# Kernel optimization log

Hardware: AMD Instinct MI355X
Metric: run time of the kernel (lower is better)

Reference implementation:

```python
import jax, jax.numpy as jnp
import numpy as np

N_HEADS, N_LEVELS, N_POINTS, D_MODEL = 8, 3, 12, 64
PARAM_NAMES = ['vp0_w','vp0_b','vp1_w','vp1_b','so0_w','so0_b','so1_w','so1_b','so2_w','so2_b','so3_w','so3_b','aw0_w','aw0_b','aw1_w','aw1_b','aw2_w','aw2_b','aw3_w','aw3_b','op0_w','op0_b','op1_w','op1_b']

def _lrelu(x):
    return jnp.where(x >= 0, x, 0.1 * x)

def _conv(x, w, b):
    y = jax.lax.conv_general_dilated(x, w, (1, 1), 'SAME', dimension_numbers=('NCHW', 'OIHW', 'NCHW'))
    return y + b[None, :, None, None]

def _bilinear(img, px, py):
    # img [B,C,H,W]; px,py [B,Q] absolute pixel coords; zero padding (grid_sample 'zeros')
    B, C, H, W = img.shape
    flat = img.reshape(B, C, H * W)
    x0 = jnp.floor(px); y0 = jnp.floor(py)
    wx1 = px - x0; wy1 = py - y0
    def g(xi, yi, wgt):
        valid = (xi >= 0) & (xi <= W - 1) & (yi >= 0) & (yi <= H - 1)
        xi_c = jnp.clip(xi, 0, W - 1).astype(jnp.int32)
        yi_c = jnp.clip(yi, 0, H - 1).astype(jnp.int32)
        v = jnp.take_along_axis(flat, (yi_c * W + xi_c)[:, None, :], axis=2)
        return v * (wgt * valid)[:, None, :]
    return (g(x0, y0, (1 - wx1) * (1 - wy1)) + g(x0 + 1, y0, wx1 * (1 - wy1))
          + g(x0, y0 + 1, (1 - wx1) * wy1) + g(x0 + 1, y0 + 1, wx1 * wy1))

def _flow_warp(img, flow):
    # img [n,C,h,w]; flow [n,2,h,w] (x,y); matches grid_sample align_corners=True
    n, C, h, w = img.shape
    gy, gx = jnp.meshgrid(jnp.arange(h, dtype=img.dtype), jnp.arange(w, dtype=img.dtype), indexing='ij')
    px = (gx[None] + flow[:, 0]).reshape(n, h * w)
    py = (gy[None] + flow[:, 1]).reshape(n, h * w)
    return _bilinear(img, px, py).reshape(n, C, h, w)

def _forward(x, flow_1, flow_2, flip_flow_1, flip_flow_2, p):
    n, t, c, h, w = x.shape
    hw = h * w; THW = t * hw
    M, L, P, D = N_HEADS, N_LEVELS, N_POINTS, c // N_HEADS
    flow_cn1 = flow_1
    flow_cn2 = flow_1 + _flow_warp(flow_2, flow_1)
    flow_n1c, flow_n1n2 = flip_flow_1, flow_2
    flow_n2n1 = flip_flow_2
    flow_n2c = flip_flow_2 + _flow_warp(flip_flow_1, flip_flow_2)
    warp_cn1 = _flow_warp(x[:, 1], flow_cn1)
    warp_cn2 = _flow_warp(x[:, 2], flow_cn2)
    warp_n1c = _flow_warp(x[:, 0], flow_n1c)
    warp_n1n2 = _flow_warp(x[:, 2], flow_n1n2)
    warp_n2n1 = _flow_warp(x[:, 1], flow_n2n1)
    warp_n2c = _flow_warp(x[:, 0], flow_n2c)
    extra = jnp.concatenate([x[:, 0], warp_cn1, warp_cn2, warp_n1c, warp_n1n2, warp_n2n1, warp_n2c,
                             flow_cn1, flow_cn2, flow_n1c, flow_n1n2, flow_n2n1, flow_n2c], axis=1)
    value = _conv(_lrelu(_conv(x.reshape(n, t * c, h, w), p['vp0_w'], p['vp0_b'])), p['vp1_w'], p['vp1_b'])
    def head(e, pre):
        y = _lrelu(_conv(e, p[pre + '0_w'], p[pre + '0_b']))
        y = _lrelu(_conv(y, p[pre + '1_w'], p[pre + '1_b']))
        y = _lrelu(_conv(y, p[pre + '2_w'], p[pre + '2_b']))
        return _conv(y, p[pre + '3_w'], p[pre + '3_b'])
    so = head(extra, 'so')  # [n, L*M*L*P*2, h, w]
    aw = head(extra, 'aw')  # [n, L*M*L*P*9, h, w]
    so = so.reshape(n, t, -1, hw).transpose(0, 1, 3, 2).reshape(n, THW, M, L, P, 2)
    aw = aw.reshape(n, t, -1, hw).transpose(0, 1, 3, 2).reshape(n, THW, M, L * P * 9)
    aw = jax.nn.softmax(aw, axis=-1).reshape(n, THW, M, L, P * 9)
    # flow-guided offsets: add per-(query-frame, target-level) flow to learned offsets
    off = so.reshape(n, t, hw, M, L, P, 2)
    fz = jnp.zeros_like(flow_cn2)
    def lvl(f0, f1, f2):
        s = jnp.stack([f0, f1, f2], 1)  # [n,3,2,h,w]
        return s.transpose(0, 3, 4, 1, 2).reshape(n, hw, L, 2)[:, None, :, None, :, None, :]
    off = jnp.concatenate([
        off[:, 0:1] + lvl(fz, flow_cn1, flow_cn2),
        off[:, 1:2] + lvl(flow_n1c, fz, flow_n1n2),
        off[:, 2:3] + lvl(flow_n2c, flow_n2n1, fz)], axis=1).reshape(n, THW, M, L, P, 2)
    # 3x3 integer patch around each sampling point
    pi, pj = jnp.meshgrid(jnp.arange(-1, 2), jnp.arange(-1, 2), indexing='ij')
    patch = jnp.stack([pi, pj], -1).reshape(1, 1, 1, 1, 1, 9, 2).astype(off.dtype)
    off = (off[..., None, :] + patch).reshape(n, THW, M, L, P * 9, 2)
    # reference points (valid_ratios are all 1: full masks are zeros)
    ry, rx = jnp.meshgrid((jnp.arange(h) + 0.5) / h, (jnp.arange(w) + 0.5) / w, indexing='ij')
    ref = jnp.stack([rx, ry], -1).reshape(1, hw, 2).astype(off.dtype)
    ref = jnp.tile(ref, (1, t, 1))  # [1, THW, 2]
    norm = jnp.array([w, h], dtype=off.dtype)
    loc = ref[:, :, None, None, None, :] + off / norm  # [n,THW,M,L,P*9,2] normalized
    # multi-scale deformable attention (all L levels share (h,w)); align_corners=False, zeros pad
    P9 = P * 9
    v = value.reshape(n, t, c, hw).transpose(0, 1, 3, 2).reshape(n, THW, M, D)
    vl = v.reshape(n, L, hw, M, D).transpose(0, 3, 1, 4, 2).reshape(n * M * L, D, h, w)
    px = (loc[..., 0] * w - 0.5).transpose(0, 2, 3, 1, 4).reshape(n * M * L, THW * P9)
    py = (loc[..., 1] * h - 0.5).transpose(0, 2, 3, 1, 4).reshape(n * M * L, THW * P9)
    sampled = _bilinear(vl, px, py).reshape(n, M, L, D, THW, P9)
    out = jnp.einsum('nmldqp,nqmlp->nqmd', sampled, aw).reshape(n, THW, c)
    out = out.reshape(n, t, h, w, c).transpose(0, 1, 4, 2, 3).reshape(n, t * c, h, w)
    out = _conv(_lrelu(_conv(out, p['op0_w'], p['op0_b'])), p['op1_w'], p['op1_b'])
    return out.reshape(n, t, c, h, w) + x

def setup_inputs():
    key = jax.random.key(0)
    n, t, c, h, w = 1, 3, 64, 32, 32
    ks = jax.random.split(key, 24)
    d = {}
    d['x'] = jax.random.normal(ks[0], (n, t, c, h, w), jnp.float32)
    for i, name in enumerate(['flow_1', 'flow_2', 'flip_flow_1', 'flip_flow_2']):
        d[name] = jax.random.normal(ks[1 + i], (n, 2, h, w), jnp.float32)
    cin_extra = 7 * c + 12
    specs = [('vp0', t * c, t * c), ('vp1', t * c, t * c),
             ('so0', c, cin_extra), ('so1', c, c), ('so2', c, c), ('so3', N_LEVELS * N_HEADS * N_LEVELS * N_POINTS * 2, c),
             ('aw0', c, cin_extra), ('aw1', c, c), ('aw2', c, c), ('aw3', N_LEVELS * N_HEADS * N_LEVELS * N_POINTS * 9, c),
             ('op0', t * c, t * c), ('op1', t * c, t * c)]
    for i, (name, co, ci) in enumerate(specs):
        kw, kb = jax.random.split(ks[5 + i])
        std = (2.0 / (ci * 9)) ** 0.5
        d[name + '_w'] = jax.random.normal(kw, (co, ci, 3, 3), jnp.float32) * std
        d[name + '_b'] = jax.random.normal(kb, (co,), jnp.float32) * 0.01
    return d

def reference(x, flow_1, flow_2, flip_flow_1, flip_flow_2, vp0_w, vp0_b, vp1_w, vp1_b, so0_w, so0_b, so1_w, so1_b, so2_w, so2_b, so3_w, so3_b, aw0_w, aw0_b, aw1_w, aw1_b, aw2_w, aw2_b, aw3_w, aw3_b, op0_w, op0_b, op1_w, op1_b):
    p = dict(zip(PARAM_NAMES, (vp0_w, vp0_b, vp1_w, vp1_b, so0_w, so0_b, so1_w, so1_b, so2_w, so2_b, so3_w, so3_b, aw0_w, aw0_b, aw1_w, aw1_b, aw2_w, aw2_b, aw3_w, aw3_b, op0_w, op0_b, op1_w, op1_b)))
    return _forward(x, flow_1, flow_2, flip_flow_1, flip_flow_2, p)
```

## Files before the change

### kernel.cpp

```cpp
#include <hip/hip_runtime.h>
#include <math.h>

#define HW 1024

typedef __attribute__((ext_vector_type(8))) short bf16x8;
typedef __attribute__((ext_vector_type(4))) float floatx4;

__device__ __forceinline__ unsigned short f2bf(float f) {
    unsigned u = __float_as_uint(f);
    u += 0x7FFF + ((u >> 16) & 1);
    return (unsigned short)(u >> 16);
}
__device__ __forceinline__ float bf2f(unsigned short u) {
    return __uint_as_float(((unsigned)u) << 16);
}
__device__ __forceinline__ float bflo(unsigned u) { return __uint_as_float(u << 16); }
__device__ __forceinline__ float bfhi(unsigned u) { return __uint_as_float(u & 0xffff0000u); }

__device__ __forceinline__ float bilin32(const float* __restrict__ img, float px, float py) {
    float x0f = floorf(px), y0f = floorf(py);
    float wx = px - x0f, wy = py - y0f;
    bool vx0 = (x0f >= 0.f) && (x0f <= 31.f);
    bool vx1 = (x0f >= -1.f) && (x0f <= 30.f);
    bool vy0 = (y0f >= 0.f) && (y0f <= 31.f);
    bool vy1 = (y0f >= -1.f) && (y0f <= 30.f);
    int ix0 = (int)fminf(fmaxf(x0f, 0.f), 31.f);
    int iy0 = (int)fminf(fmaxf(y0f, 0.f), 31.f);
    int ix1 = (int)fminf(fmaxf(x0f + 1.f, 0.f), 31.f);
    int iy1 = (int)fminf(fmaxf(y0f + 1.f, 0.f), 31.f);
    float w00 = (1.f - wx) * (1.f - wy) * ((vx0 && vy0) ? 1.f : 0.f);
    float w01 = wx * (1.f - wy) * ((vx1 && vy0) ? 1.f : 0.f);
    float w10 = (1.f - wx) * wy * ((vx0 && vy1) ? 1.f : 0.f);
    float w11 = wx * wy * ((vx1 && vy1) ? 1.f : 0.f);
    return w00 * img[iy0 * 32 + ix0] + w01 * img[iy0 * 32 + ix1] +
           w10 * img[iy1 * 32 + ix0] + w11 * img[iy1 * 32 + ix1];
}

__device__ __forceinline__ float2 comp_flow(const float* __restrict__ fa,
                                            const float* __restrict__ fb, int pix) {
    int y = pix >> 5, x = pix & 31;
    float fx = fa[pix], fy = fa[HW + pix];
    float px = (float)x + fx, py = (float)y + fy;
    float2 r;
    r.x = fx + bilin32(fb, px, py);
    r.y = fy + bilin32(fb + HW, px, py);
    return r;
}

struct WD { const float* src; int cout, Cin, nCb, wbase, beg; };

__device__ __forceinline__ void wxform_tile(const WD w, int local,
                                            unsigned short* __restrict__ wgt, char* smraw) {
    float* wlds = (float*)smraw;
    const int tid = threadIdx.x;
    int co16 = local / w.nCb, cb = local - co16 * w.nCb;
    int cr0 = co16 * 16, ci0 = cb * 32;
    for (int i = tid; i < 16 * 288; i += 256) {
        int cr = i / 288, o = i - cr * 288;
        int crg = cr0 + cr, ci = ci0 + o / 9;
        float v = (crg < w.cout && ci < w.Cin)
            ? w.src[((size_t)crg * w.Cin + ci0) * 9 + o] : 0.f;
        wlds[i] = v;
    }
    __syncthreads();
    for (int e = tid; e < 9 * 512; e += 256) {
        int t = e >> 9, idx = e & 511;
        int j = idx & 7, lane = idx >> 3, q = lane >> 4, mm = lane & 15;
        wgt[((size_t)w.wbase + ((size_t)co16 * 9 + t) * w.nCb + cb) * 512 + idx] =
            f2bf(wlds[mm * 288 + (q * 8 + j) * 9 + t]);
    }
}

struct PrepP {
    const float *x, *f1, *f2, *ff1, *ff2;
    float *fcn2, *fn2c;
    unsigned short *x_pad, *extra_pad, *wgt;
    WD wd[4];
};

__global__ __launch_bounds__(256) void prep_k(PrepP P) {
    __shared__ __align__(16) char sm[16 * 288 * 4];
    const int b = blockIdx.x, tid = threadIdx.x;
    if (b < 192) {
        int idx = b * 256 + tid;
        int pix = idx / 48, c4 = idx - pix * 48;
        int y = pix >> 5, xx = pix & 31;
        int c0 = c4 * 4;
        ushort4 s;
        s.x = f2bf(P.x[(size_t)(c0 + 0) * HW + pix]);
        s.y = f2bf(P.x[(size_t)(c0 + 1) * HW + pix]);
        s.z = f2bf(P.x[(size_t)(c0 + 2) * HW + pix]);
        s.w = f2bf(P.x[(size_t)(c0 + 3) * HW + pix]);
        *(ushort4*)(&P.x_pad[(size_t)((y + 1) * 34 + xx + 1) * 192 + c0]) = s;
    } else if (b < 672) {
        int idx = (b - 192) * 256 + tid;
        int pix = idx / 120, c4 = idx - pix * 120;
        int y = pix >> 5, xx = pix & 31;
        int c0 = c4 * 4;
        float va[4];
        if (c0 < 64) {
#pragma unroll
            for (int k = 0; k < 4; ++k) va[k] = P.x[(size_t)(c0 + k) * HW + pix];
        } else if (c0 < 448) {
            int grp = (c0 - 64) >> 6;
            int c = (c0 - 64) & 63;
            const float* src; float fx, fy;
            if (grp == 0)      { src = P.x + 64 * HW;  fx = P.f1[pix];  fy = P.f1[HW + pix]; }
            else if (grp == 1) { src = P.x + 128 * HW; float2 r = comp_flow(P.f1, P.f2, pix);  fx = r.x; fy = r.y; }
            else if (grp == 2) { src = P.x;            fx = P.ff1[pix]; fy = P.ff1[HW + pix]; }
            else if (grp == 3) { src = P.x + 128 * HW; fx = P.f2[pix];  fy = P.f2[HW + pix]; }
            else if (grp == 4) { src = P.x + 64 * HW;  fx = P.ff2[pix]; fy = P.ff2[HW + pix]; }
            else               { src = P.x;            float2 r = comp_flow(P.ff2, P.ff1, pix); fx = r.x; fy = r.y; }
            float px = (float)xx + fx, py = (float)y + fy;
            float x0f = floorf(px), y0f = floorf(py);
            float wx = px - x0f, wy = py - y0f;
            bool vx0 = (x0f >= 0.f) && (x0f <= 31.f);
            bool vx1 = (x0f >= -1.f) && (x0f <= 30.f);
            bool vy0 = (y0f >= 0.f) && (y0f <= 31.f);
            bool vy1 = (y0f >= -1.f) && (y0f <= 30.f);
            int ix0 = (int)fminf(fmaxf(x0f, 0.f), 31.f);
            int iy0 = (int)fminf(fmaxf(y0f, 0.f), 31.f);
            int ix1 = (int)fminf(fmaxf(x0f + 1.f, 0.f), 31.f);
            int iy1 = (int)fminf(fmaxf(y0f + 1.f, 0.f), 31.f);
            float w00 = (1.f - wx) * (1.f - wy) * ((vx0 && vy0) ? 1.f : 0.f);
            float w01 = wx * (1.f - wy) * ((vx1 && vy0) ? 1.f : 0.f);
            float w10 = (1.f - wx) * wy * ((vx0 && vy1) ? 1.f : 0.f);
            float w11 = wx * wy * ((vx1 && vy1) ? 1.f : 0.f);
            int p00 = iy0 * 32 + ix0, p01 = iy0 * 32 + ix1;
            int p10 = iy1 * 32 + ix0, p11 = iy1 * 32 + ix1;
            const float* im = src + (size_t)c * HW;
#pragma unroll
            for (int k = 0; k < 4; ++k) {
                va[k] = w00 * im[p00] + w01 * im[p01] + w10 * im[p10] + w11 * im[p11];
                im += HW;
            }
        } else {
#pragma unroll
            for (int k = 0; k < 4; ++k) {
                int ch = c0 + k;
                float v = 0.f;
                if (ch < 460) {
                    int fc = ch - 448;
                    int which = fc >> 1, comp = fc & 1;
                    if (which == 0)      v = P.f1[comp * HW + pix];
                    else if (which == 1) { float2 r = comp_flow(P.f1, P.f2, pix);  v = comp ? r.y : r.x; }
                    else if (which == 2) v = P.ff1[comp * HW + pix];
                    else if (which == 3) v = P.f2[comp * HW + pix];
                    else if (which == 4) v = P.ff2[comp * HW + pix];
                    else                 { float2 r = comp_flow(P.ff2, P.ff1, pix); v = comp ? r.y : r.x; }
                }
                va[k] = v;
            }
        }
        ushort4 s;
        s.x = f2bf(va[0]); s.y = f2bf(va[1]); s.z = f2bf(va[2]); s.w = f2bf(va[3]);
        *(ushort4*)(&P.extra_pad[(size_t)((y + 1) * 34 + xx + 1) * 480 + c0]) = s;
    } else if (b < 688) {
        int idx = (b - 672) * 256 + tid;
        if (idx < 1024) {
            float2 r = comp_flow(P.f1, P.f2, idx);
            P.fcn2[idx] = r.x; P.fcn2[HW + idx] = r.y;
        } else if (idx < 2048) {
            int pix = idx - 1024;
            float2 r = comp_flow(P.ff2, P.ff1, pix);
            P.fn2c[pix] = r.x; P.fn2c[HW + pix] = r.y;
        }
    } else if (b < 704) {
        const int chans[9] = {192, 192, 480, 64, 64, 64, 64, 192, 192};
        size_t offs[9]; size_t a = 0;
        for (int i = 0; i < 9; ++i) { offs[i] = a; a += (size_t)1156 * chans[i]; }
        int bb = b - 688;
        for (int item = bb; item < 9 * 132; item += 16) {
            int buf = item / 132, i = item - buf * 132;
            int py, px;
            if (i < 34) { py = 0; px = i; }
            else if (i < 68) { py = 33; px = i - 34; }
            else { int j = i - 68; py = 1 + (j >> 1); px = (j & 1) ? 33 : 0; }
            int C = chans[buf];
            unsigned short* p = P.x_pad + offs[buf] + (size_t)(py * 34 + px) * C;
            for (int c = tid; c < C; c += 256) p[c] = 0;
        }
    } else {
        int blk = b - 704;
        int di = 0;
        while (di < 3 && blk >= P.wd[di + 1].beg) ++di;
        wxform_tile(P.wd[di], blk - P.wd[di].beg, P.wgt, sm);
    }
}

struct CDesc {
    const unsigned short* in;
    const unsigned short* wgt;
    const float* bias;
    void* out;
    const float* residual;
    int Cpad, nCb, Cout, mode, cmod, relu, Mblocks;
};
struct CParam {
    CDesc d[4];
    WD rwd[4];
    int rbeg[5];
    int nr;
    int ride_bx0;
    unsigned short* wgt;
};

template<int PIXROWS, int COBLK>
__device__ __forceinline__ void conv_tile(const CDesc d, int bx, int by, char* smraw) {
    constexpr int TROWS = PIXROWS + 2;
    constexpr int TC = TROWS * 34 * 4;
    constexpr int ITRIPS = (TC + 255) / 256;
    constexpr int NTY = PIXROWS / 4;
    constexpr int NACC = NTY * 2;
    constexpr int MT = COBLK / 16;
    constexpr int WN = MT * 9 * 64;
    constexpr int WTRIPS = (WN + 255) / 256;
    unsigned short* blds = (unsigned short*)smraw;
    unsigned short* wlds = (unsigned short*)(smraw + TROWS * 34 * 40 * 2);

    const int tid = threadIdx.x;
    const int w = tid >> 6, lane = tid & 63;
    const int lq = lane >> 4, ln = lane & 15;
    const int co0 = bx * COBLK;
    const int y0 = by * PIXROWS;
    const unsigned short* __restrict__ in = d.in;
    const unsigned short* __restrict__ wg = d.wgt;
    const int Cpad = d.Cpad, nCb = d.nCb;

    floatx4 acc[MT][NACC];
#pragma unroll
    for (int mt = 0; mt < MT; ++mt)
#pragma unroll
        for (int nt = 0; nt < NACC; ++nt)
            acc[mt][nt] = (floatx4){0.f, 0.f, 0.f, 0.f};

    bf16x8 ireg[ITRIPS];
    bf16x8 wreg[WTRIPS];

    auto load_regs = [&](int cb) {
        const int ci0 = cb << 5;
#pragma unroll
        for (int k = 0; k < ITRIPS; ++k) {
            int i = tid + k * 256;
            if (i < TC) {
                int r = i / 136, rem = i - r * 136, c = rem >> 2, g = rem & 3;
                ireg[k] = *(const bf16x8*)(in + (size_t)((y0 + r) * 34 + c) * Cpad + ci0 + g * 8);
            }
        }
#pragma unroll
        for (int k = 0; k < WTRIPS; ++k) {
            int i = tid + k * 256;
            if (i < WN) {
                int chunk = i >> 6, l16 = i & 63;
                int mt = chunk / 9, t = chunk - mt * 9;
                wreg[k] = *(const bf16x8*)(wg + ((size_t)(((co0 >> 4) + mt) * 9 + t) * nCb + cb) * 512 + l16 * 8);
            }
        }
    };

    load_regs(0);

    for (int cb = 0; cb < nCb; ++cb) {
        __syncthreads();
#pragma unroll
        for (int k = 0; k < ITRIPS; ++k) {
            int i = tid + k * 256;
            if (i < TC) {
                int r = i / 136, rem = i - r * 136, c = rem >> 2, g = rem & 3;
                *(bf16x8*)(&blds[(r * 34 + c) * 40 + g * 8]) = ireg[k];
            }
        }
#pragma unroll
        for (int k = 0; k < WTRIPS; ++k) {
            int i = tid + k * 256;
            if (i < WN) {
                int chunk = i >> 6, l16 = i & 63;
                *(bf16x8*)(&wlds[chunk * 512 + l16 * 8]) = wreg[k];
            }
        }
        __syncthreads();
        if (cb + 1 < nCb) load_regs(cb + 1);
        for (int t = 0; t < 9; ++t) {
            const int dy = t / 3, dx = t - dy * 3;
            bf16x8 bfr[NACC];
#pragma unroll
            for (int ty = 0; ty < NTY; ++ty)
#pragma unroll
                for (int tx = 0; tx < 2; ++tx) {
                    int yy = w * NTY + ty + dy;
                    int xx = tx * 16 + ln + dx;
                    bfr[ty * 2 + tx] = *(const bf16x8*)(&blds[(yy * 34 + xx) * 40 + lq * 8]);
                }
#pragma unroll
            for (int mt = 0; mt < MT; ++mt) {
                bf16x8 afr = *(const bf16x8*)(&wlds[(mt * 9 + t) * 512 + lane * 8]);
#pragma unroll
                for (int nt = 0; nt < NACC; ++nt)
                    acc[mt][nt] = __builtin_amdgcn_mfma_f32_16x16x32_bf16(afr, bfr[nt], acc[mt][nt], 0, 0, 0);
            }
        }
    }

#pragma unroll
    for (int mt = 0; mt < MT; ++mt) {
        const int co = co0 + mt * 16 + lq * 4;
        if (co >= d.Cout) continue;
        float bv[4];
#pragma unroll
        for (int r = 0; r < 4; ++r) bv[r] = d.bias[co + r];
#pragma unroll
        for (int nt = 0; nt < NACC; ++nt) {
            const int ty = nt >> 1, tx = nt & 1;
            const int pix = by * (PIXROWS * 32) + (w * NTY + ty) * 32 + tx * 16 + ln;
            float v[4];
#pragma unroll
            for (int r = 0; r < 4; ++r) {
                float vv = acc[mt][nt][r] + bv[r];
                if (d.relu) vv = (vv >= 0.f) ? vv : 0.1f * vv;
                v[r] = vv;
            }
            if (d.mode == 0) {
                float* o = (float*)d.out;
#pragma unroll
                for (int r = 0; r < 4; ++r) {
                    float vv = v[r];
                    if (d.residual) vv += d.residual[(size_t)(co + r) * HW + pix];
                    o[(size_t)(co + r) * HW + pix] = vv;
                }
            } else if (d.mode == 1) {
                int fq = co / d.cmod, cc = co - fq * d.cmod;
                *(float4*)((float*)d.out + ((size_t)fq * HW + pix) * d.cmod + cc) =
                    make_float4(v[0], v[1], v[2], v[3]);
            } else if (d.mode == 2) {
                int fq = co / d.cmod, cc = co - fq * d.cmod;
                ushort4 s4;
                s4.x = f2bf(v[0]); s4.y = f2bf(v[1]); s4.z = f2bf(v[2]); s4.w = f2bf(v[3]);
                *(ushort4*)((unsigned short*)d.out + ((size_t)fq * HW + pix) * d.cmod + cc) = s4;
            } else {
                int yy = (pix >> 5) + 1, xx = (pix & 31) + 1;
                ushort4 s4;
                s4.x = f2bf(v[0]); s4.y = f2bf(v[1]); s4.z = f2bf(v[2]); s4.w = f2bf(v[3]);
                *(ushort4*)((unsigned short*)d.out + (size_t)(yy * 34 + xx) * d.cmod + co) = s4;
            }
        }
    }
}

template<int PIXROWS, int COBLK>
__global__ __launch_bounds__(256) void conv_mfma_k(CParam P) {
    constexpr int TROWS = PIXROWS + 2;
    constexpr int MT = COBLK / 16;
    constexpr int SMB = TROWS * 34 * 40 * 2 + MT * 9 * 512 * 2;
    __shared__ __align__(16) char sm[(SMB > 18432) ? SMB : 18432];
    int bx = blockIdx.x;
    if (P.nr > 0 && bx >= P.ride_bx0) {
        int slot = (bx - P.ride_bx0) * gridDim.y + blockIdx.y;
        if (slot >= P.rbeg[P.nr]) return;
        int di = 0;
        while (di + 1 < P.nr && slot >= P.rbeg[di + 1]) ++di;
        wxform_tile(P.rwd[di], slot - P.rbeg[di], P.wgt, sm);
        return;
    }
    int di = 0;
    while (bx >= P.d[di].Mblocks) { bx -= P.d[di].Mblocks; ++di; }
    conv_tile<PIXROWS, COBLK>(P.d[di], bx, blockIdx.y, sm);
}

__global__ __launch_bounds__(256) void deform_attn_k(
    const unsigned short* __restrict__ value_b, const float* __restrict__ so_t,
    const unsigned short* __restrict__ aw_t,
    const float* __restrict__ flow_1, const float* __restrict__ flow_2,
    const float* __restrict__ flip_flow_1, const float* __restrict__ flip_flow_2,
    const float* __restrict__ flow_cn2, const float* __restrict__ flow_n2c,
    unsigned short* __restrict__ attn_pad)
{
    __shared__ unsigned short vlds[24576];
    __shared__ unsigned short pwlds[4][432];
    const int tid = threadIdx.x;
    const int wav = tid >> 6, lane = tid & 63;
    const int m = blockIdx.x & 7, qc = blockIdx.x >> 3;

    for (int i = tid; i < 3072; i += 256) {
        int l = i >> 10, p = i & 1023;
        *(bf16x8*)(&vlds[(size_t)i * 8]) =
            *(const bf16x8*)(value_b + ((size_t)((l * 8 + m) * 1024) + p) * 8);
    }
    __syncthreads();

    const int pp = lane & 15, gq = lane >> 4;
    const int gdy = (gq >> 1) * 2 - 1;
    const int gdx = (gq & 1) * 2 - 1;
    const bool selx = (gq & 1);
    const bool sely = (gq >> 1);

    float av[6];
    {
        const unsigned short* awp = aw_t + (size_t)(qc * 32 + wav) * 2592 + m * 324;
#pragma unroll
        for (int it = 0; it < 6; ++it) {
            int j = lane + it * 64;
            av[it] = (j < 324) ? bf2f(awp[j]) : -1e30f;
        }
    }

    for (int r = 0; r < 8; ++r) {
        const int q = qc * 32 + r * 4 + wav;
        const int f = q >> 10, pix = q & 1023;
        const int y = pix >> 5, x = pix & 31;

        const float* sop = so_t + (size_t)q * 576 + m * 72;
        float2 so2r[3];
#pragma unroll
        for (int pt = 0; pt < 3; ++pt) {
            int pi = pt * 16 + pp;
            if (pi < 36) so2r[pt] = *(const float2*)(sop + pi * 2);
            else { so2r[pt].x = 0.f; so2r[pt].y = 0.f; }
        }

        float flx0 = 0.f, fly0 = 0.f, flx1 = 0.f, fly1 = 0.f, flx2 = 0.f, fly2 = 0.f;
        if (f == 0) {
            flx1 = flow_1[pix];      fly1 = flow_1[HW + pix];
            flx2 = flow_cn2[pix];    fly2 = flow_cn2[HW + pix];
        } else if (f == 1) {
            flx0 = flip_flow_1[pix]; fly0 = flip_flow_1[HW + pix];
            flx2 = flow_2[pix];      fly2 = flow_2[HW + pix];
        } else {
            flx0 = flow_n2c[pix];    fly0 = flow_n2c[HW + pix];
            flx1 = flip_flow_2[pix]; fly1 = flip_flow_2[HW + pix];
        }

        float vmax = -1e30f;
#pragma unroll
        for (int it = 0; it < 6; ++it) vmax = fmaxf(vmax, av[it]);
#pragma unroll
        for (int off = 32; off; off >>= 1) vmax = fmaxf(vmax, __shfl_xor(vmax, off));
        float ssum = 0.f;
#pragma unroll
        for (int it = 0; it < 6; ++it) {
            int j = lane + it * 64;
            float e = (j < 324) ? __expf(av[it] - vmax) : 0.f;
            av[it] = e;
            ssum += e;
        }
#pragma unroll
        for (int off = 32; off; off >>= 1) ssum += __shfl_xor(ssum, off);
        const float inv = 1.f / ssum;

#pragma unroll
        for (int it = 0; it < 6; ++it) {
            int j = lane + it * 64;
            if (j < 324) {
                int pi = j / 9, k = j - pi * 9;
                pwlds[wav][pi * 12 + k] = f2bf(av[it] * inv);
            }
        }

        float avn[6];
        if (r < 7) {
            const unsigned short* awn = aw_t + (size_t)(q + 4) * 2592 + m * 324;
#pragma unroll
            for (int it = 0; it < 6; ++it) {
                int j = lane + it * 64;
                avn[it] = (j < 324) ? bf2f(awn[j]) : -1e30f;
            }
        }

        float acc[8];
#pragma unroll
        for (int dd = 0; dd < 8; ++dd) acc[dd] = 0.f;

#pragma unroll
        for (int pt = 0; pt < 3; ++pt) {
            int pi = pt * 16 + pp;
            if (pi < 36) {
                int l = pi / 12;
                float2 so2 = so2r[pt];
                float fx = (l == 0) ? flx0 : (l == 1) ? flx1 : flx2;
                float fy = (l == 0) ? fly0 : (l == 1) ? fly1 : fly2;
                float bxf = (float)x + so2.x + fx;
                float byf = (float)y + so2.y + fy;
                float x0f = floorf(bxf), y0f = floorf(byf);
                float wx = bxf - x0f, wy = byf - y0f;
                float ax = 1.f - wx, ay = 1.f - wy;
                int x0 = (int)fminf(fmaxf(x0f, -2.f), 34.f);
                int y0 = (int)fminf(fmaxf(y0f, -2.f), 34.f);

                const unsigned short* pr = &pwlds[wav][pi * 12];
                uint2 pv0 = *(const uint2*)(pr);
                uint2 pv1 = *(const uint2*)(pr + 4);
                float a0 = bflo(pv0.x), a1 = bfhi(pv0.x), a2 = bflo(pv0.y);
                float a3 = bfhi(pv0.y), a4 = bflo(pv1.x), a5 = bfhi(pv1.x);
                float a6 = bflo(pv1.y), a7 = bfhi(pv1.y), a8 = bf2f(pr[8]);

                float bs0a, bs0b, bs1a, bs1b, bs2a, bs2b;
                {
                    float b0, b1, b2, b3;
                    b0 = a0 * ax; b1 = a0 * wx + a3 * ax; b2 = a3 * wx + a6 * ax; b3 = a6 * wx;
                    bs0a = selx ? b2 : b0; bs0b = selx ? b3 : b1;
                    b0 = a1 * ax; b1 = a1 * wx + a4 * ax; b2 = a4 * wx + a7 * ax; b3 = a7 * wx;
                    bs1a = selx ? b2 : b0; bs1b = selx ? b3 : b1;
                    b0 = a2 * ax; b1 = a2 * wx + a5 * ax; b2 = a5 * wx + a8 * ax; b3 = a8 * wx;
                    bs2a = selx ? b2 : b0; bs2b = selx ? b3 : b1;
                }
                float c00, c01, c10, c11;
                {
                    float c0 = bs0a * ay, c1 = bs0a * wy + bs1a * ay;
                    float c2 = bs1a * wy + bs2a * ay, c3 = bs2a * wy;
                    c00 = sely ? c2 : c0; c10 = sely ? c3 : c1;
                    c0 = bs0b * ay; c1 = bs0b * wy + bs1b * ay;
                    c2 = bs1b * wy + bs2b * ay; c3 = bs2b * wy;
                    c01 = sely ? c2 : c0; c11 = sely ? c3 : c1;
                }
                float cg[2][2] = {{c00, c01}, {c10, c11}};
                const int vbase = l * 1024;
#pragma unroll
                for (int sy = 0; sy < 2; ++sy) {
#pragma unroll
                    for (int sx = 0; sx < 2; ++sx) {
                        int dy = gdy + sy, dx = gdx + sx;
                        float pyf = y0f + (float)dy, pxf = x0f + (float)dx;
                        bool v = (pxf >= 0.f) && (pxf <= 31.f) && (pyf >= 0.f) && (pyf <= 31.f);
                        int px = min(max(x0 + dx, 0), 31);
                        int py = min(max(y0 + dy, 0), 31);
                        float c = cg[sy][sx] * (v ? 1.f : 0.f);
                        uint4 vv = *(const uint4*)(&vlds[(size_t)(vbase + py * 32 + px) * 8]);
                        acc[0] = fmaf(c, bflo(vv.x), acc[0]);
                        acc[1] = fmaf(c, bfhi(vv.x), acc[1]);
                        acc[2] = fmaf(c, bflo(vv.y), acc[2]);
                        acc[3] = fmaf(c, bfhi(vv.y), acc[3]);
                        acc[4] = fmaf(c, bflo(vv.z), acc[4]);
                        acc[5] = fmaf(c, bfhi(vv.z), acc[5]);
                        acc[6] = fmaf(c, bflo(vv.w), acc[6]);
                        acc[7] = fmaf(c, bfhi(vv.w), acc[7]);
                    }
                }
            }
        }

#pragma unroll
        for (int dd = 0; dd < 8; ++dd) {
#pragma unroll
            for (int off = 32; off; off >>= 1) acc[dd] += __shfl_xor(acc[dd], off);
        }
        if (lane == 0) {
            unsigned short* op = attn_pad + (size_t)((y + 1) * 34 + x + 1) * 192 + f * 64 + m * 8;
            ushort4 s0, s1;
            s0.x = f2bf(acc[0]); s0.y = f2bf(acc[1]); s0.z = f2bf(acc[2]); s0.w = f2bf(acc[3]);
            s1.x = f2bf(acc[4]); s1.y = f2bf(acc[5]); s1.z = f2bf(acc[6]); s1.w = f2bf(acc[7]);
            *(ushort4*)(op) = s0;
            *(ushort4*)(op + 4) = s1;
        }
        if (r < 7) {
#pragma unroll
            for (int it = 0; it < 6; ++it) av[it] = avn[it];
        }
    }
}

extern "C" void kernel_launch(void* const* d_in, const int* in_sizes, int n_in,
                              void* d_out, int out_size, void* d_ws, size_t ws_size,
                              hipStream_t stream) {
    const float* x      = (const float*)d_in[0];
    const float* flow_1 = (const float*)d_in[1];
    const float* flow_2 = (const float*)d_in[2];
    const float* flip_1 = (const float*)d_in[3];
    const float* flip_2 = (const float*)d_in[4];
    const float* vp0_w = (const float*)d_in[5];  const float* vp0_b = (const float*)d_in[6];
    const float* vp1_w = (const float*)d_in[7];  const float* vp1_b = (const float*)d_in[8];
    const float* so0_w = (const float*)d_in[9];  const float* so0_b = (const float*)d_in[10];
    const float* so1_w = (const float*)d_in[11]; const float* so1_b = (const float*)d_in[12];
    const float* so2_w = (const float*)d_in[13]; const float* so2_b = (const float*)d_in[14];
    const float* so3_w = (const float*)d_in[15]; const float* so3_b = (const float*)d_in[16];
    const float* aw0_w = (const float*)d_in[17]; const float* aw0_b = (const float*)d_in[18];
    const float* aw1_w = (const float*)d_in[19]; const float* aw1_b = (const float*)d_in[20];
    const float* aw2_w = (const float*)d_in[21]; const float* aw2_b = (const float*)d_in[22];
    const float* aw3_w = (const float*)d_in[23]; const float* aw3_b = (const float*)d_in[24];
    const float* op0_w = (const float*)d_in[25]; const float* op0_b = (const float*)d_in[26];
    const float* op1_w = (const float*)d_in[27]; const float* op1_b = (const float*)d_in[28];
    float* out = (float*)d_out;
    (void)ws_size; (void)in_sizes; (void)n_in; (void)out_size;

    float* fws = (float*)d_ws;
    float* flow_cn2 = fws;
    float* flow_n2c = flow_cn2 + 2048;
    unsigned short* value_b = (unsigned short*)(flow_n2c + 2048);
    float* so_t     = (float*)(value_b + 196608);
    unsigned short* uws = (unsigned short*)(so_t + 1769472);
    unsigned short* x_pad     = uws;
    unsigned short* vp0h      = x_pad + 1156 * 192;
    unsigned short* extra_pad = vp0h + 1156 * 192;
    unsigned short* s1 = extra_pad + 1156 * 480;
    unsigned short* a1 = s1 + 1156 * 64;
    unsigned short* s2 = a1 + 1156 * 64;
    unsigned short* a2 = s2 + 1156 * 64;
    unsigned short* attn_pad = a2 + 1156 * 64;
    unsigned short* op0h     = attn_pad + 1156 * 192;
    unsigned short* aw_t = op0h + 1156 * 192;
    unsigned short* wgt  = aw_t + (size_t)3072 * 2592;

    PrepP pp;
    pp.x = x; pp.f1 = flow_1; pp.f2 = flow_2; pp.ff1 = flip_1; pp.ff2 = flip_2;
    pp.fcn2 = flow_cn2; pp.fn2c = flow_n2c;
    pp.x_pad = x_pad; pp.extra_pad = extra_pad; pp.wgt = wgt;
    pp.wd[0] = {vp0_w, 192, 192, 6,     0,   0};
    pp.wd[1] = {vp1_w, 192, 192, 6,   648,  72};
    pp.wd[2] = {so0_w,  64, 460, 15, 1296, 144};
    pp.wd[3] = {aw0_w,  64, 460, 15, 1836, 204};
    prep_k<<<968, 256, 0, stream>>>(pp);

    const int BIG = 1 << 30;
    CDesc nul = {nullptr, nullptr, nullptr, nullptr, nullptr, 0, 0, 0, 0, 0, 0, BIG};
    WD wnul = {nullptr, 0, 0, 1, 0, 0};

    {
        CParam cp;
        cp.d[0] = {x_pad,     wgt + (size_t)0 * 512,    vp0_b, vp0h, nullptr, 192, 6,  192, 3, 192, 1, 12};
        cp.d[1] = {extra_pad, wgt + (size_t)1296 * 512, so0_b, s1,   nullptr, 480, 15, 64,  3, 64,  1, 4};
        cp.d[2] = {extra_pad, wgt + (size_t)1836 * 512, aw0_b, a1,   nullptr, 480, 15, 64,  3, 64,  1, 4};
        cp.d[3] = nul;
        cp.rwd[0] = {so1_w, 64, 64, 2, 2376, 0};
        cp.rwd[1] = {aw1_w, 64, 64, 2, 2448, 0};
        cp.rwd[2] = {so2_w, 64, 64, 2, 2520, 0};
        cp.rwd[3] = {aw2_w, 64, 64, 2, 2592, 0};
        cp.rbeg[0] = 0; cp.rbeg[1] = 8; cp.rbeg[2] = 16; cp.rbeg[3] = 24; cp.rbeg[4] = 32;
        cp.nr = 4; cp.ride_bx0 = 20; cp.wgt = wgt;
        conv_mfma_k<4, 16><<<dim3(24, 8), 256, 0, stream>>>(cp);
    }
    {
        CParam cp;
        cp.d[0] = {vp0h, wgt + (size_t)648 * 512,  vp1_b, value_b, nullptr, 192, 6, 192, 2, 8,  0, 12};
        cp.d[1] = {s1,   wgt + (size_t)2376 * 512, so1_b, s2,      nullptr, 64,  2, 64,  3, 64, 1, 4};
        cp.d[2] = {a1,   wgt + (size_t)2448 * 512, aw1_b, a2,      nullptr, 64,  2, 64,  3, 64, 1, 4};
        cp.d[3] = nul;
        cp.rwd[0] = {so3_w, 1728, 64, 2, 2664, 0};
        cp.rwd[1] = {aw3_w, 7776, 64, 2, 4608, 0};
        cp.rwd[2] = wnul; cp.rwd[3] = wnul;
        cp.rbeg[0] = 0; cp.rbeg[1] = 216; cp.rbeg[2] = 1188; cp.rbeg[3] = 1188; cp.rbeg[4] = 1188;
        cp.nr = 2; cp.ride_bx0 = 20; cp.wgt = wgt;
        conv_mfma_k<4, 16><<<dim3(169, 8), 256, 0, stream>>>(cp);
    }
    {
        CParam cp;
        cp.d[0] = {s2, wgt + (size_t)2520 * 512, so2_b, s1, nullptr, 64, 2, 64, 3, 64, 1, 4};
        cp.d[1] = {a2, wgt + (size_t)2592 * 512, aw2_b, a1, nullptr, 64, 2, 64, 3, 64, 1, 4};
        cp.d[2] = nul; cp.d[3] = nul;
        cp.rwd[0] = {op0_w, 192, 192, 6, 13392, 0};
        cp.rwd[1] = {op1_w, 192, 192, 6, 14040, 0};
        cp.rwd[2] = wnul; cp.rwd[3] = wnul;
        cp.rbeg[0] = 0; cp.rbeg[1] = 72; cp.rbeg[2] = 144; cp.rbeg[3] = 144; cp.rbeg[4] = 144;
        cp.nr = 2; cp.ride_bx0 = 8; cp.wgt = wgt;
        conv_mfma_k<4, 16><<<dim3(26, 8), 256, 0, stream>>>(cp);
    }
    {
        CParam cp;
        cp.d[0] = {s1, wgt + (size_t)2664 * 512, so3_b, so_t, nullptr, 64, 2, 1728, 1, 576,  0, 27};
        cp.d[1] = {a1, wgt + (size_t)4608 * 512, aw3_b, aw_t, nullptr, 64, 2, 7776, 2, 2592, 0, 122};
        cp.d[2] = nul; cp.d[3] = nul;
        cp.nr = 0; cp.ride_bx0 = BIG; cp.wgt = wgt;
        cp.rwd[0] = wnul; cp.rwd[1] = wnul; cp.rwd[2] = wnul; cp.rwd[3] = wnul;
        cp.rbeg[0] = 0; cp.rbeg[1] = 0; cp.rbeg[2] = 0; cp.rbeg[3] = 0; cp.rbeg[4] = 0;
        conv_mfma_k<8, 64><<<dim3(149, 4), 256, 0, stream>>>(cp);
    }

    deform_attn_k<<<768, 256, 0, stream>>>(value_b, so_t, aw_t,
                                           flow_1, flow_2, flip_1, flip_2,
                                           flow_cn2, flow_n2c, attn_pad);

    {
        CParam cp;
        cp.d[0] = {attn_pad, wgt + (size_t)13392 * 512, op0_b, op0h, nullptr, 192, 6, 192, 3, 192, 1, 12};
        cp.d[1] = nul; cp.d[2] = nul; cp.d[3] = nul;
        cp.nr = 0; cp.ride_bx0 = BIG; cp.wgt = wgt;
        cp.rwd[0] = wnul; cp.rwd[1] = wnul; cp.rwd[2] = wnul; cp.rwd[3] = wnul;
        cp.rbeg[0] = 0; cp.rbeg[1] = 0; cp.rbeg[2] = 0; cp.rbeg[3] = 0; cp.rbeg[4] = 0;
        conv_mfma_k<4, 16><<<dim3(12, 8), 256, 0, stream>>>(cp);
    }
    {
        CParam cp;
        cp.d[0] = {op0h, wgt + (size_t)14040 * 512, op1_b, out, x, 192, 6, 192, 0, 0, 0, 12};
        cp.d[1] = nul; cp.d[2] = nul; cp.d[3] = nul;
        cp.nr = 0; cp.ride_bx0 = BIG; cp.wgt = wgt;
        cp.rwd[0] = wnul; cp.rwd[1] = wnul; cp.rwd[2] = wnul; cp.rwd[3] = wnul;
        cp.rbeg[0] = 0; cp.rbeg[1] = 0; cp.rbeg[2] = 0; cp.rbeg[3] = 0; cp.rbeg[4] = 0;
        conv_mfma_k<4, 16><<<dim3(12, 8), 256, 0, stream>>>(cp);
    }
}
```

Measured before the change: 281.9 us.

## Move all weight transforms into prep kernel instead of riding conv launches

Weight reformatting (fp32 OIHW to bf16 MFMA tile layout) for all twelve conv layers now runs in the single prep kernel, which grows from 968 to 2336 blocks. Before, eight of these transforms were spread across later conv launches as extra 'ride-along' blocks. The conv kernel loses its ride-along dispatch and uses statically sized shared arrays. Launch grids shrink to the real conv work, so later stages finish sooner, but prep becomes longer and overlaps less work.

Result: faster. 266.5 us (-5.5%).

```diff
diff --git a/kernel.cpp b/kernel.cpp
--- a/kernel.cpp
+++ b/kernel.cpp
@@ -48,38 +48,15 @@
 }
 
 struct WD { const float* src; int cout, Cin, nCb, wbase, beg; };
-
-__device__ __forceinline__ void wxform_tile(const WD w, int local,
-                                            unsigned short* __restrict__ wgt, char* smraw) {
-    float* wlds = (float*)smraw;
-    const int tid = threadIdx.x;
-    int co16 = local / w.nCb, cb = local - co16 * w.nCb;
-    int cr0 = co16 * 16, ci0 = cb * 32;
-    for (int i = tid; i < 16 * 288; i += 256) {
-        int cr = i / 288, o = i - cr * 288;
-        int crg = cr0 + cr, ci = ci0 + o / 9;
-        float v = (crg < w.cout && ci < w.Cin)
-            ? w.src[((size_t)crg * w.Cin + ci0) * 9 + o] : 0.f;
-        wlds[i] = v;
-    }
-    __syncthreads();
-    for (int e = tid; e < 9 * 512; e += 256) {
-        int t = e >> 9, idx = e & 511;
-        int j = idx & 7, lane = idx >> 3, q = lane >> 4, mm = lane & 15;
-        wgt[((size_t)w.wbase + ((size_t)co16 * 9 + t) * w.nCb + cb) * 512 + idx] =
-            f2bf(wlds[mm * 288 + (q * 8 + j) * 9 + t]);
-    }
-}
-
 struct PrepP {
     const float *x, *f1, *f2, *ff1, *ff2;
     float *fcn2, *fn2c;
     unsigned short *x_pad, *extra_pad, *wgt;
-    WD wd[4];
+    WD wd[12];
 };
 
 __global__ __launch_bounds__(256) void prep_k(PrepP P) {
-    __shared__ __align__(16) char sm[16 * 288 * 4];
+    __shared__ float wlds[16 * 288];
     const int b = blockIdx.x, tid = threadIdx.x;
     if (b < 192) {
         int idx = b * 256 + tid;
@@ -183,8 +160,25 @@
     } else {
         int blk = b - 704;
         int di = 0;
-        while (di < 3 && blk >= P.wd[di + 1].beg) ++di;
-        wxform_tile(P.wd[di], blk - P.wd[di].beg, P.wgt, sm);
+        while (di < 11 && blk >= P.wd[di + 1].beg) ++di;
+        WD w = P.wd[di];
+        int local = blk - w.beg;
+        int co16 = local / w.nCb, cb = local - co16 * w.nCb;
+        int cr0 = co16 * 16, ci0 = cb * 32;
+        for (int i = tid; i < 16 * 288; i += 256) {
+            int cr = i / 288, o = i - cr * 288;
+            int crg = cr0 + cr, ci = ci0 + o / 9;
+            float v = (crg < w.cout && ci < w.Cin)
+                ? w.src[((size_t)crg * w.Cin + ci0) * 9 + o] : 0.f;
+            wlds[i] = v;
+        }
+        __syncthreads();
+        for (int e = tid; e < 9 * 512; e += 256) {
+            int t = e >> 9, idx = e & 511;
+            int j = idx & 7, lane = idx >> 3, q = lane >> 4, mm = lane & 15;
+            P.wgt[((size_t)w.wbase + ((size_t)co16 * 9 + t) * w.nCb + cb) * 512 + idx] =
+                f2bf(wlds[mm * 288 + (q * 8 + j) * 9 + t]);
+        }
     }
 }
 
@@ -196,17 +190,10 @@
     const float* residual;
     int Cpad, nCb, Cout, mode, cmod, relu, Mblocks;
 };
-struct CParam {
-    CDesc d[4];
-    WD rwd[4];
-    int rbeg[5];
-    int nr;
-    int ride_bx0;
-    unsigned short* wgt;
-};
+struct CParam { CDesc d[4]; };
 
 template<int PIXROWS, int COBLK>
-__device__ __forceinline__ void conv_tile(const CDesc d, int bx, int by, char* smraw) {
+__global__ __launch_bounds__(256) void conv_mfma_k(CParam P) {
     constexpr int TROWS = PIXROWS + 2;
     constexpr int TC = TROWS * 34 * 4;
     constexpr int ITRIPS = (TC + 255) / 256;
@@ -215,14 +202,19 @@
     constexpr int MT = COBLK / 16;
     constexpr int WN = MT * 9 * 64;
     constexpr int WTRIPS = (WN + 255) / 256;
-    unsigned short* blds = (unsigned short*)smraw;
-    unsigned short* wlds = (unsigned short*)(smraw + TROWS * 34 * 40 * 2);
+    __shared__ unsigned short blds[TROWS * 34 * 40];
+    __shared__ unsigned short wlds[MT * 9 * 512];
+
+    int bx = blockIdx.x;
+    int di = 0;
+    while (bx >= P.d[di].Mblocks) { bx -= P.d[di].Mblocks; ++di; }
+    const CDesc d = P.d[di];
 
     const int tid = threadIdx.x;
     const int w = tid >> 6, lane = tid & 63;
     const int lq = lane >> 4, ln = lane & 15;
     const int co0 = bx * COBLK;
-    const int y0 = by * PIXROWS;
+    const int by = blockIdx.y, y0 = by * PIXROWS;
     const unsigned short* __restrict__ in = d.in;
     const unsigned short* __restrict__ wg = d.wgt;
     const int Cpad = d.Cpad, nCb = d.nCb;
@@ -344,26 +336,6 @@
             }
         }
     }
-}
-
-template<int PIXROWS, int COBLK>
-__global__ __launch_bounds__(256) void conv_mfma_k(CParam P) {
-    constexpr int TROWS = PIXROWS + 2;
-    constexpr int MT = COBLK / 16;
-    constexpr int SMB = TROWS * 34 * 40 * 2 + MT * 9 * 512 * 2;
-    __shared__ __align__(16) char sm[(SMB > 18432) ? SMB : 18432];
-    int bx = blockIdx.x;
-    if (P.nr > 0 && bx >= P.ride_bx0) {
-        int slot = (bx - P.ride_bx0) * gridDim.y + blockIdx.y;
-        if (slot >= P.rbeg[P.nr]) return;
-        int di = 0;
-        while (di + 1 < P.nr && slot >= P.rbeg[di + 1]) ++di;
-        wxform_tile(P.rwd[di], slot - P.rbeg[di], P.wgt, sm);
-        return;
-    }
-    int di = 0;
-    while (bx >= P.d[di].Mblocks) { bx -= P.d[di].Mblocks; ++di; }
-    conv_tile<PIXROWS, COBLK>(P.d[di], bx, blockIdx.y, sm);
 }
 
 __global__ __launch_bounds__(256) void deform_attn_k(
@@ -602,15 +574,22 @@
     pp.x = x; pp.f1 = flow_1; pp.f2 = flow_2; pp.ff1 = flip_1; pp.ff2 = flip_2;
     pp.fcn2 = flow_cn2; pp.fn2c = flow_n2c;
     pp.x_pad = x_pad; pp.extra_pad = extra_pad; pp.wgt = wgt;
-    pp.wd[0] = {vp0_w, 192, 192, 6,     0,   0};
-    pp.wd[1] = {vp1_w, 192, 192, 6,   648,  72};
-    pp.wd[2] = {so0_w,  64, 460, 15, 1296, 144};
-    pp.wd[3] = {aw0_w,  64, 460, 15, 1836, 204};
-    prep_k<<<968, 256, 0, stream>>>(pp);
+    pp.wd[0]  = {vp0_w, 192, 192, 6,     0,    0};
+    pp.wd[1]  = {vp1_w, 192, 192, 6,   648,   72};
+    pp.wd[2]  = {so0_w,  64, 460, 15, 1296,  144};
+    pp.wd[3]  = {aw0_w,  64, 460, 15, 1836,  204};
+    pp.wd[4]  = {so1_w,  64,  64, 2,  2376,  264};
+    pp.wd[5]  = {aw1_w,  64,  64, 2,  2448,  272};
+    pp.wd[6]  = {so2_w,  64,  64, 2,  2520,  280};
+    pp.wd[7]  = {aw2_w,  64,  64, 2,  2592,  288};
+    pp.wd[8]  = {so3_w, 1728, 64, 2,  2664,  296};
+    pp.wd[9]  = {aw3_w, 7776, 64, 2,  4608,  512};
+    pp.wd[10] = {op0_w, 192, 192, 6, 13392, 1488};
+    pp.wd[11] = {op1_w, 192, 192, 6, 14040, 1560};
+    prep_k<<<2336, 256, 0, stream>>>(pp);
 
     const int BIG = 1 << 30;
     CDesc nul = {nullptr, nullptr, nullptr, nullptr, nullptr, 0, 0, 0, 0, 0, 0, BIG};
-    WD wnul = {nullptr, 0, 0, 1, 0, 0};
 
     {
         CParam cp;
@@ -618,13 +597,7 @@
         cp.d[1] = {extra_pad, wgt + (size_t)1296 * 512, so0_b, s1,   nullptr, 480, 15, 64,  3, 64,  1, 4};
         cp.d[2] = {extra_pad, wgt + (size_t)1836 * 512, aw0_b, a1,   nullptr, 480, 15, 64,  3, 64,  1, 4};
         cp.d[3] = nul;
-        cp.rwd[0] = {so1_w, 64, 64, 2, 2376, 0};
-        cp.rwd[1] = {aw1_w, 64, 64, 2, 2448, 0};
-        cp.rwd[2] = {so2_w, 64, 64, 2, 2520, 0};
-        cp.rwd[3] = {aw2_w, 64, 64, 2, 2592, 0};
-        cp.rbeg[0] = 0; cp.rbeg[1] = 8; cp.rbeg[2] = 16; cp.rbeg[3] = 24; cp.rbeg[4] = 32;
-        cp.nr = 4; cp.ride_bx0 = 20; cp.wgt = wgt;
-        conv_mfma_k<4, 16><<<dim3(24, 8), 256, 0, stream>>>(cp);
+        conv_mfma_k<4, 16><<<dim3(20, 8), 256, 0, stream>>>(cp);
     }
     {
         CParam cp;
@@ -632,33 +605,20 @@
         cp.d[1] = {s1,   wgt + (size_t)2376 * 512, so1_b, s2,      nullptr, 64,  2, 64,  3, 64, 1, 4};
         cp.d[2] = {a1,   wgt + (size_t)2448 * 512, aw1_b, a2,      nullptr, 64,  2, 64,  3, 64, 1, 4};
         cp.d[3] = nul;
-        cp.rwd[0] = {so3_w, 1728, 64, 2, 2664, 0};
-        cp.rwd[1] = {aw3_w, 7776, 64, 2, 4608, 0};
-        cp.rwd[2] = wnul; cp.rwd[3] = wnul;
-        cp.rbeg[0] = 0; cp.rbeg[1] = 216; cp.rbeg[2] = 1188; cp.rbeg[3] = 1188; cp.rbeg[4] = 1188;
-        cp.nr = 2; cp.ride_bx0 = 20; cp.wgt = wgt;
-        conv_mfma_k<4, 16><<<dim3(169, 8), 256, 0, stream>>>(cp);
+        conv_mfma_k<4, 16><<<dim3(20, 8), 256, 0, stream>>>(cp);
     }
     {
         CParam cp;
         cp.d[0] = {s2, wgt + (size_t)2520 * 512, so2_b, s1, nullptr, 64, 2, 64, 3, 64, 1, 4};
         cp.d[1] = {a2, wgt + (size_t)2592 * 512, aw2_b, a1, nullptr, 64, 2, 64, 3, 64, 1, 4};
         cp.d[2] = nul; cp.d[3] = nul;
-        cp.rwd[0] = {op0_w, 192, 192, 6, 13392, 0};
-        cp.rwd[1] = {op1_w, 192, 192, 6, 14040, 0};
-        cp.rwd[2] = wnul; cp.rwd[3] = wnul;
-        cp.rbeg[0] = 0; cp.rbeg[1] = 72; cp.rbeg[2] = 144; cp.rbeg[3] = 144; cp.rbeg[4] = 144;
-        cp.nr = 2; cp.ride_bx0 = 8; cp.wgt = wgt;
-        conv_mfma_k<4, 16><<<dim3(26, 8), 256, 0, stream>>>(cp);
+        conv_mfma_k<4, 16><<<dim3(8, 8), 256, 0, stream>>>(cp);
     }
     {
         CParam cp;
         cp.d[0] = {s1, wgt + (size_t)2664 * 512, so3_b, so_t, nullptr, 64, 2, 1728, 1, 576,  0, 27};
         cp.d[1] = {a1, wgt + (size_t)4608 * 512, aw3_b, aw_t, nullptr, 64, 2, 7776, 2, 2592, 0, 122};
         cp.d[2] = nul; cp.d[3] = nul;
-        cp.nr = 0; cp.ride_bx0 = BIG; cp.wgt = wgt;
-        cp.rwd[0] = wnul; cp.rwd[1] = wnul; cp.rwd[2] = wnul; cp.rwd[3] = wnul;
-        cp.rbeg[0] = 0; cp.rbeg[1] = 0; cp.rbeg[2] = 0; cp.rbeg[3] = 0; cp.rbeg[4] = 0;
         conv_mfma_k<8, 64><<<dim3(149, 4), 256, 0, stream>>>(cp);
     }
 
@@ -670,18 +630,12 @@
         CParam cp;
         cp.d[0] = {attn_pad, wgt + (size_t)13392 * 512, op0_b, op0h, nullptr, 192, 6, 192, 3, 192, 1, 12};
         cp.d[1] = nul; cp.d[2] = nul; cp.d[3] = nul;
-        cp.nr = 0; cp.ride_bx0 = BIG; cp.wgt = wgt;
-        cp.rwd[0] = wnul; cp.rwd[1] = wnul; cp.rwd[2] = wnul; cp.rwd[3] = wnul;
-        cp.rbeg[0] = 0; cp.rbeg[1] = 0; cp.rbeg[2] = 0; cp.rbeg[3] = 0; cp.rbeg[4] = 0;
         conv_mfma_k<4, 16><<<dim3(12, 8), 256, 0, stream>>>(cp);
     }
     {
         CParam cp;
         cp.d[0] = {op0h, wgt + (size_t)14040 * 512, op1_b, out, x, 192, 6, 192, 0, 0, 0, 12};
         cp.d[1] = nul; cp.d[2] = nul; cp.d[3] = nul;
-        cp.nr = 0; cp.ride_bx0 = BIG; cp.wgt = wgt;
-        cp.rwd[0] = wnul; cp.rwd[1] = wnul; cp.rwd[2] = wnul; cp.rwd[3] = wnul;
-        cp.rbeg[0] = 0; cp.rbeg[1] = 0; cp.rbeg[2] = 0; cp.rbeg[3] = 0; cp.rbeg[4] = 0;
         conv_mfma_k<4, 16><<<dim3(12, 8), 256, 0, stream>>>(cp);
     }
 }
```
